# Kernel optimization log

Measured on AMD Instinct MI355X. Metric: run time of the kernel, lower is better.

Reference implementation:

```python
import jax, jax.numpy as jnp
import numpy as np

EPS = 1e-7  # K.epsilon()
ROUTINGS = 3
NUM_CAPSULE = 8
FILTERS = 16


def squash(v, axis=-1):
    s2 = jnp.sum(jnp.square(v), axis=axis, keepdims=True)
    scale = s2 / (1.0 + s2) / jnp.sqrt(s2 + EPS)
    return scale * v


def _conv_per_caps(x, w):
    # x: [B,H,W,Cin], w: [k,k,Cin,Cout]
    return jax.lax.conv_general_dilated(
        x, w, window_strides=(1, 1), padding='SAME',
        dimension_numbers=('NHWC', 'HWIO', 'NHWC'))


def setup_inputs() -> dict:
    key = jax.random.key(0)
    k1, k2 = jax.random.split(key, 2)
    B, H, Wd, IN_CAPS, IN_F = 32, 32, 32, 8, 16
    input_tensor = jax.random.normal(k1, (B, H, Wd, IN_CAPS, IN_F), dtype=jnp.float32)
    # he_normal fan_in = k*k*Cin = 3*3*16 = 144
    W = jax.random.normal(k2, (IN_CAPS, 3, 3, IN_F, NUM_CAPSULE * FILTERS), dtype=jnp.float32) * np.sqrt(2.0 / 144.0)
    b = jnp.full((1, 1, NUM_CAPSULE, FILTERS), 0.1, dtype=jnp.float32)
    return {"input_tensor": input_tensor, "W": W, "b": b}


def reference(input_tensor, W, b):
    B, H, Wd, in_caps, in_f = input_tensor.shape
    # per-input-capsule conv: vmap over capsule axis of input and weight
    votes = jax.vmap(_conv_per_caps, in_axes=(3, 0), out_axes=1)(input_tensor, W)
    # [B, in_caps, H, W, num_cap*F] -> [B, in_caps, H, W, num_cap, F]
    votes = votes.reshape(B, in_caps, H, Wd, NUM_CAPSULE, FILTERS)

    # dynamic routing
    logits = jnp.zeros((B, in_caps, H, Wd, NUM_CAPSULE), dtype=votes.dtype)
    activation = None
    for i in range(ROUTINGS):
        route = jax.nn.softmax(logits, axis=-1)  # over output capsules
        # sum over input capsules of route-weighted votes, plus bias
        preactivate = jnp.einsum('bihwc,bihwcf->bhwcf', route, votes) + b
        activation = squash(preactivate, axis=-1)
        if i < ROUTINGS - 1:
            # scalar-product agreement
            logits = logits + jnp.einsum('bihwcf,bhwcf->bihwc', votes, activation)
    return activation.astype(jnp.float32)
```

## Files before the change

### kernel.cpp

```cpp
#include <hip/hip_runtime.h>
#include <math.h>


typedef _Float16 fp16x8 __attribute__((ext_vector_type(8)));
typedef float f32x4 __attribute__((ext_vector_type(4)));

#define EPS 1e-7f
constexpr int PSTRIDE = 136;
constexpr int PCOLS   = 34;
constexpr int PROWS   = 4;
constexpr int LSTRIDE = 76;
constexpr int PXS     = 76;
constexpr int W_ELEMS = 40 * 8 * 64 * 8;

__device__ __forceinline__ float sumquad(float v) {
    v += __shfl_xor(v, 16);
    v += __shfl_xor(v, 32);
    return v;
}

__global__ __launch_bounds__(256)
void prep_weights(const float* __restrict__ wts,
                  _Float16* __restrict__ w16) {
    int n = blockIdx.x * 256 + threadIdx.x;
    if (n >= W_ELEMS) return;
    int j    = n & 7;
    int ln   = (n >> 3) & 63;
    int c0   = (n >> 9) & 7;
    int iq   = n >> 12;
    int i0   = iq / 5;
    int q0   = iq - i0 * 5;
    int k = q0 * 32 + (ln >> 4) * 8 + j;
    float w = 0.f;
    if (k < 144) w = wts[(i0 * 144 + k) * 128 + c0 * 16 + (ln & 15)];
    w16[n] = (_Float16)w;
}

__global__ __launch_bounds__(1024, 4)
void capsule_mfma_kernel(const float* __restrict__ x,
                         const _Float16* __restrict__ w16,
                         const float* __restrict__ bias,
                         float* __restrict__ out)
{
    __shared__ _Float16 patch[PROWS * PCOLS * PSTRIDE];
    __shared__ float lg_arr[64 * LSTRIDE];
    __shared__ float r_arr[64 * PXS];

    const int tid  = threadIdx.x;
    const int lane = tid & 63;
    const int w    = tid >> 6;
    const int c    = w & 7;
    const int g    = w >> 3;
    const int l15  = lane & 15;
    const int quad = lane >> 4;
    const int lane8 = lane * 8;

    const int bid = blockIdx.x;
    const int h2 = bid & 15, b = bid >> 4;
    const int h = h2 << 1;

    const float4* x4 = (const float4*)x;
    for (int idx = tid; idx < PROWS * PCOLS * 32; idx += 1024) {
        int ch4  = idx & 31;
        int slot = idx >> 5;
        int row  = slot / PCOLS;
        int colp = slot - row * PCOLS;
        int gh = h - 1 + row;
        int gw = colp - 1;
        float4 v = {0.f, 0.f, 0.f, 0.f};
        if ((unsigned)gh < 32u && (unsigned)gw < 32u)
            v = x4[(((b * 32 + gh) * 32 + gw) << 5) + ch4];
        _Float16 ph[4];
        ph[0] = (_Float16)v.x; ph[1] = (_Float16)v.y;
        ph[2] = (_Float16)v.z; ph[3] = (_Float16)v.w;
        *(ushort4*)&patch[slot * PSTRIDE + ch4 * 4] = *(const ushort4*)ph;
    }
    __syncthreads();

    int a_off[5];
    #pragma unroll
    for (int q = 0; q < 5; ++q) {
        int tap = 2 * q + (quad >> 1);
        if (tap > 8) tap = 8;
        int dy = tap / 3, dx = tap - dy * 3;
        a_off[q] = ((g + dy) * PCOLS + l15 + dx) * PSTRIDE + (quad & 1) * 8;
    }

    f32x4 acc[2][8];
    #pragma unroll
    for (int mt = 0; mt < 2; ++mt)
        #pragma unroll
        for (int i = 0; i < 8; ++i) acc[mt][i] = (f32x4){0.f, 0.f, 0.f, 0.f};

    #pragma unroll
    for (int q = 0; q < 5; ++q) {
        #pragma unroll
        for (int i = 0; i < 8; ++i) {
            int woff = ((i * 5 + q) * 8 + c) * 512 + lane8;
            fp16x8 aw = *(const fp16x8*)(w16 + woff);
            fp16x8 b0 = *(const fp16x8*)(patch + a_off[q] + i * 16);
            fp16x8 b1 = *(const fp16x8*)(patch + a_off[q] + 16 * PSTRIDE + i * 16);
            acc[0][i] = __builtin_amdgcn_mfma_f32_16x16x32_f16(aw, b0, acc[0][i], 0, 0, 0);
            acc[1][i] = __builtin_amdgcn_mfma_f32_16x16x32_f16(aw, b1, acc[1][i], 0, 0, 0);
        }
    }

    const float4 bb4 = *(const float4*)(bias + c * 16 + quad * 4);
    const float barr[4] = {bb4.x, bb4.y, bb4.z, bb4.w};

    float actv[2][4];

    #pragma unroll
    for (int mt = 0; mt < 2; ++mt) {
        float pre[4];
        #pragma unroll
        for (int r = 0; r < 4; ++r) {
            float s = acc[mt][0][r] + acc[mt][1][r] + acc[mt][2][r] + acc[mt][3][r]
                    + acc[mt][4][r] + acc[mt][5][r] + acc[mt][6][r] + acc[mt][7][r];
            pre[r] = s * 0.125f + barr[r];
        }
        float s2 = sumquad(pre[0]*pre[0] + pre[1]*pre[1] + pre[2]*pre[2] + pre[3]*pre[3]);
        float scale = s2 * __builtin_amdgcn_rsqf(s2 + EPS) * __builtin_amdgcn_rcpf(1.f + s2);
        #pragma unroll
        for (int r = 0; r < 4; ++r) actv[mt][r] = scale * pre[r];
    }
    #pragma unroll
    for (int mt = 0; mt < 2; ++mt) {
        int slot = g * 32 + mt * 16 + l15;
        #pragma unroll
        for (int i = 0; i < 8; ++i) {
            float t = acc[mt][i][0]*actv[mt][0] + acc[mt][i][1]*actv[mt][1]
                    + acc[mt][i][2]*actv[mt][2] + acc[mt][i][3]*actv[mt][3];
            t = sumquad(t);
            if (quad == 0) lg_arr[slot * LSTRIDE + i * 9 + c] = t;
        }
    }
    __syncthreads();
    if (tid < 512) {
        int p = tid >> 3, ii = tid & 7;
        const float* lrow = &lg_arr[p * LSTRIDE + ii * 9];
        float m = lrow[0];
        #pragma unroll
        for (int cc = 1; cc < 8; ++cc) m = fmaxf(m, lrow[cc]);
        float e[8]; float den = 0.f;
        #pragma unroll
        for (int cc = 0; cc < 8; ++cc) { e[cc] = __expf(lrow[cc] - m); den += e[cc]; }
        float rd = __builtin_amdgcn_rcpf(den);
        #pragma unroll
        for (int cc = 0; cc < 8; ++cc) r_arr[p * PXS + cc * 8 + ii] = e[cc] * rd;
    }
    __syncthreads();

    #pragma unroll
    for (int mt = 0; mt < 2; ++mt) {
        int slot = g * 32 + mt * 16 + l15;
        const float4* rp = (const float4*)&r_arr[slot * PXS + c * 8];
        float4 r0 = rp[0], r1 = rp[1];
        float pre[4];
        #pragma unroll
        for (int r = 0; r < 4; ++r) {
            float s;
            s  = r0.x * acc[mt][0][r]; s = fmaf(r0.y, acc[mt][1][r], s);
            s  = fmaf(r0.z, acc[mt][2][r], s); s = fmaf(r0.w, acc[mt][3][r], s);
            s  = fmaf(r1.x, acc[mt][4][r], s); s = fmaf(r1.y, acc[mt][5][r], s);
            s  = fmaf(r1.z, acc[mt][6][r], s); s = fmaf(r1.w, acc[mt][7][r], s);
            pre[r] = s + barr[r];
        }
        float s2 = sumquad(pre[0]*pre[0] + pre[1]*pre[1] + pre[2]*pre[2] + pre[3]*pre[3]);
        float scale = s2 * __builtin_amdgcn_rsqf(s2 + EPS) * __builtin_amdgcn_rcpf(1.f + s2);
        #pragma unroll
        for (int r = 0; r < 4; ++r) actv[mt][r] = scale * pre[r];
    }
    #pragma unroll
    for (int mt = 0; mt < 2; ++mt) {
        int slot = g * 32 + mt * 16 + l15;
        #pragma unroll
        for (int i = 0; i < 8; ++i) {
            float t = acc[mt][i][0]*actv[mt][0] + acc[mt][i][1]*actv[mt][1]
                    + acc[mt][i][2]*actv[mt][2] + acc[mt][i][3]*actv[mt][3];
            t = sumquad(t);
            if (quad == 0) lg_arr[slot * LSTRIDE + i * 9 + c] += t;
        }
    }
    __syncthreads();
    if (tid < 512) {
        int p = tid >> 3, ii = tid & 7;
        const float* lrow = &lg_arr[p * LSTRIDE + ii * 9];
        float m = lrow[0];
        #pragma unroll
        for (int cc = 1; cc < 8; ++cc) m = fmaxf(m, lrow[cc]);
        float e[8]; float den = 0.f;
        #pragma unroll
        for (int cc = 0; cc < 8; ++cc) { e[cc] = __expf(lrow[cc] - m); den += e[cc]; }
        float rd = __builtin_amdgcn_rcpf(den);
        #pragma unroll
        for (int cc = 0; cc < 8; ++cc) r_arr[p * PXS + cc * 8 + ii] = e[cc] * rd;
    }
    __syncthreads();

    #pragma unroll
    for (int mt = 0; mt < 2; ++mt) {
        int slot = g * 32 + mt * 16 + l15;
        const float4* rp = (const float4*)&r_arr[slot * PXS + c * 8];
        float4 r0 = rp[0], r1 = rp[1];
        float pre[4];
        #pragma unroll
        for (int r = 0; r < 4; ++r) {
            float s;
            s  = r0.x * acc[mt][0][r]; s = fmaf(r0.y, acc[mt][1][r], s);
            s  = fmaf(r0.z, acc[mt][2][r], s); s = fmaf(r0.w, acc[mt][3][r], s);
            s  = fmaf(r1.x, acc[mt][4][r], s); s = fmaf(r1.y, acc[mt][5][r], s);
            s  = fmaf(r1.z, acc[mt][6][r], s); s = fmaf(r1.w, acc[mt][7][r], s);
            pre[r] = s + barr[r];
        }
        float s2 = sumquad(pre[0]*pre[0] + pre[1]*pre[1] + pre[2]*pre[2] + pre[3]*pre[3]);
        float scale = s2 * __builtin_amdgcn_rsqf(s2 + EPS) * __builtin_amdgcn_rcpf(1.f + s2);
        float4 o4 = { scale*pre[0], scale*pre[1], scale*pre[2], scale*pre[3] };
        int gh = h + g;
        int px = mt * 16 + l15;
        *(float4*)(out + (((b * 32 + gh) * 32 + px) << 7) + c * 16 + quad * 4) = o4;
    }
}

extern "C" void kernel_launch(void* const* d_in, const int* in_sizes, int n_in,
                              void* d_out, int out_size, void* d_ws, size_t ws_size,
                              hipStream_t stream) {
    const float* x    = (const float*)d_in[0];
    const float* wts  = (const float*)d_in[1];
    const float* bias = (const float*)d_in[2];
    float* out        = (float*)d_out;
    _Float16* w16     = (_Float16*)d_ws;

    prep_weights<<<dim3(640), dim3(256), 0, stream>>>(wts, w16);
    capsule_mfma_kernel<<<dim3(512), dim3(1024), 0, stream>>>(x, w16, bias, out);
}
```

Before: 102.0 us.

## Process two row-pairs per block and prefetch the next input patch into LDS

Each block now handles two consecutive row-pairs, halving the grid. While the MFMA conv and routing for the first tile run, the input patch for the second tile is loaded from global memory straight into a new fp32 LDS staging buffer with global_load_lds. That staged data is then converted to fp16 for the second pass. The extra staging buffer greatly raises LDS use, which likely drops residency to one 1024-thread block per CU and so loses the overlap that came from running two blocks at once.

```diff
diff --git a/kernel.cpp b/kernel.cpp
--- a/kernel.cpp
+++ b/kernel.cpp
@@ -9,6 +9,7 @@
 constexpr int PSTRIDE = 136;
 constexpr int PCOLS   = 34;
 constexpr int PROWS   = 4;
+constexpr int NSTG    = PROWS * PCOLS * 32;
 constexpr int LSTRIDE = 76;
 constexpr int PXS     = 76;
 constexpr int W_ELEMS = 40 * 8 * 64 * 8;
@@ -17,6 +18,12 @@
     v += __shfl_xor(v, 16);
     v += __shfl_xor(v, 32);
     return v;
+}
+
+__device__ __forceinline__ void gll16(const float4* g, float4* l) {
+    __builtin_amdgcn_global_load_lds(
+        (const __attribute__((address_space(1))) unsigned int*)(const void*)g,
+        (__attribute__((address_space(3))) unsigned int*)(void*)l, 16, 0, 0);
 }
 
 __global__ __launch_bounds__(256)
@@ -43,6 +50,7 @@
                          float* __restrict__ out)
 {
     __shared__ _Float16 patch[PROWS * PCOLS * PSTRIDE];
+    __shared__ float4 stage32[NSTG];
     __shared__ float lg_arr[64 * LSTRIDE];
     __shared__ float r_arr[64 * PXS];
 
@@ -56,26 +64,12 @@
     const int lane8 = lane * 8;
 
     const int bid = blockIdx.x;
-    const int h2 = bid & 15, b = bid >> 4;
-    const int h = h2 << 1;
+    const int t0  = bid * 2;
+    const int h2  = t0 & 15;
+    const int b   = t0 >> 4;
+    const int h0  = h2 << 1;
 
     const float4* x4 = (const float4*)x;
-    for (int idx = tid; idx < PROWS * PCOLS * 32; idx += 1024) {
-        int ch4  = idx & 31;
-        int slot = idx >> 5;
-        int row  = slot / PCOLS;
-        int colp = slot - row * PCOLS;
-        int gh = h - 1 + row;
-        int gw = colp - 1;
-        float4 v = {0.f, 0.f, 0.f, 0.f};
-        if ((unsigned)gh < 32u && (unsigned)gw < 32u)
-            v = x4[(((b * 32 + gh) * 32 + gw) << 5) + ch4];
-        _Float16 ph[4];
-        ph[0] = (_Float16)v.x; ph[1] = (_Float16)v.y;
-        ph[2] = (_Float16)v.z; ph[3] = (_Float16)v.w;
-        *(ushort4*)&patch[slot * PSTRIDE + ch4 * 4] = *(const ushort4*)ph;
-    }
-    __syncthreads();
 
     int a_off[5];
     #pragma unroll
@@ -86,139 +80,194 @@
         a_off[q] = ((g + dy) * PCOLS + l15 + dx) * PSTRIDE + (quad & 1) * 8;
     }
 
-    f32x4 acc[2][8];
-    #pragma unroll
-    for (int mt = 0; mt < 2; ++mt)
-        #pragma unroll
-        for (int i = 0; i < 8; ++i) acc[mt][i] = (f32x4){0.f, 0.f, 0.f, 0.f};
-
-    #pragma unroll
-    for (int q = 0; q < 5; ++q) {
-        #pragma unroll
-        for (int i = 0; i < 8; ++i) {
-            int woff = ((i * 5 + q) * 8 + c) * 512 + lane8;
-            fp16x8 aw = *(const fp16x8*)(w16 + woff);
-            fp16x8 b0 = *(const fp16x8*)(patch + a_off[q] + i * 16);
-            fp16x8 b1 = *(const fp16x8*)(patch + a_off[q] + 16 * PSTRIDE + i * 16);
-            acc[0][i] = __builtin_amdgcn_mfma_f32_16x16x32_f16(aw, b0, acc[0][i], 0, 0, 0);
-            acc[1][i] = __builtin_amdgcn_mfma_f32_16x16x32_f16(aw, b1, acc[1][i], 0, 0, 0);
-        }
-    }
-
     const float4 bb4 = *(const float4*)(bias + c * 16 + quad * 4);
     const float barr[4] = {bb4.x, bb4.y, bb4.z, bb4.w};
 
-    float actv[2][4];
-
-    #pragma unroll
-    for (int mt = 0; mt < 2; ++mt) {
-        float pre[4];
-        #pragma unroll
-        for (int r = 0; r < 4; ++r) {
-            float s = acc[mt][0][r] + acc[mt][1][r] + acc[mt][2][r] + acc[mt][3][r]
-                    + acc[mt][4][r] + acc[mt][5][r] + acc[mt][6][r] + acc[mt][7][r];
-            pre[r] = s * 0.125f + barr[r];
-        }
-        float s2 = sumquad(pre[0]*pre[0] + pre[1]*pre[1] + pre[2]*pre[2] + pre[3]*pre[3]);
-        float scale = s2 * __builtin_amdgcn_rsqf(s2 + EPS) * __builtin_amdgcn_rcpf(1.f + s2);
-        #pragma unroll
-        for (int r = 0; r < 4; ++r) actv[mt][r] = scale * pre[r];
-    }
-    #pragma unroll
-    for (int mt = 0; mt < 2; ++mt) {
-        int slot = g * 32 + mt * 16 + l15;
-        #pragma unroll
-        for (int i = 0; i < 8; ++i) {
-            float t = acc[mt][i][0]*actv[mt][0] + acc[mt][i][1]*actv[mt][1]
-                    + acc[mt][i][2]*actv[mt][2] + acc[mt][i][3]*actv[mt][3];
-            t = sumquad(t);
-            if (quad == 0) lg_arr[slot * LSTRIDE + i * 9 + c] = t;
-        }
-    }
-    __syncthreads();
-    if (tid < 512) {
-        int p = tid >> 3, ii = tid & 7;
-        const float* lrow = &lg_arr[p * LSTRIDE + ii * 9];
-        float m = lrow[0];
-        #pragma unroll
-        for (int cc = 1; cc < 8; ++cc) m = fmaxf(m, lrow[cc]);
-        float e[8]; float den = 0.f;
-        #pragma unroll
-        for (int cc = 0; cc < 8; ++cc) { e[cc] = __expf(lrow[cc] - m); den += e[cc]; }
-        float rd = __builtin_amdgcn_rcpf(den);
-        #pragma unroll
-        for (int cc = 0; cc < 8; ++cc) r_arr[p * PXS + cc * 8 + ii] = e[cc] * rd;
-    }
-    __syncthreads();
-
-    #pragma unroll
-    for (int mt = 0; mt < 2; ++mt) {
-        int slot = g * 32 + mt * 16 + l15;
-        const float4* rp = (const float4*)&r_arr[slot * PXS + c * 8];
-        float4 r0 = rp[0], r1 = rp[1];
-        float pre[4];
-        #pragma unroll
-        for (int r = 0; r < 4; ++r) {
-            float s;
-            s  = r0.x * acc[mt][0][r]; s = fmaf(r0.y, acc[mt][1][r], s);
-            s  = fmaf(r0.z, acc[mt][2][r], s); s = fmaf(r0.w, acc[mt][3][r], s);
-            s  = fmaf(r1.x, acc[mt][4][r], s); s = fmaf(r1.y, acc[mt][5][r], s);
-            s  = fmaf(r1.z, acc[mt][6][r], s); s = fmaf(r1.w, acc[mt][7][r], s);
-            pre[r] = s + barr[r];
-        }
-        float s2 = sumquad(pre[0]*pre[0] + pre[1]*pre[1] + pre[2]*pre[2] + pre[3]*pre[3]);
-        float scale = s2 * __builtin_amdgcn_rsqf(s2 + EPS) * __builtin_amdgcn_rcpf(1.f + s2);
-        #pragma unroll
-        for (int r = 0; r < 4; ++r) actv[mt][r] = scale * pre[r];
-    }
-    #pragma unroll
-    for (int mt = 0; mt < 2; ++mt) {
-        int slot = g * 32 + mt * 16 + l15;
-        #pragma unroll
-        for (int i = 0; i < 8; ++i) {
-            float t = acc[mt][i][0]*actv[mt][0] + acc[mt][i][1]*actv[mt][1]
-                    + acc[mt][i][2]*actv[mt][2] + acc[mt][i][3]*actv[mt][3];
-            t = sumquad(t);
-            if (quad == 0) lg_arr[slot * LSTRIDE + i * 9 + c] += t;
-        }
-    }
-    __syncthreads();
-    if (tid < 512) {
-        int p = tid >> 3, ii = tid & 7;
-        const float* lrow = &lg_arr[p * LSTRIDE + ii * 9];
-        float m = lrow[0];
-        #pragma unroll
-        for (int cc = 1; cc < 8; ++cc) m = fmaxf(m, lrow[cc]);
-        float e[8]; float den = 0.f;
-        #pragma unroll
-        for (int cc = 0; cc < 8; ++cc) { e[cc] = __expf(lrow[cc] - m); den += e[cc]; }
-        float rd = __builtin_amdgcn_rcpf(den);
-        #pragma unroll
-        for (int cc = 0; cc < 8; ++cc) r_arr[p * PXS + cc * 8 + ii] = e[cc] * rd;
-    }
-    __syncthreads();
-
-    #pragma unroll
-    for (int mt = 0; mt < 2; ++mt) {
-        int slot = g * 32 + mt * 16 + l15;
-        const float4* rp = (const float4*)&r_arr[slot * PXS + c * 8];
-        float4 r0 = rp[0], r1 = rp[1];
-        float pre[4];
-        #pragma unroll
-        for (int r = 0; r < 4; ++r) {
-            float s;
-            s  = r0.x * acc[mt][0][r]; s = fmaf(r0.y, acc[mt][1][r], s);
-            s  = fmaf(r0.z, acc[mt][2][r], s); s = fmaf(r0.w, acc[mt][3][r], s);
-            s  = fmaf(r1.x, acc[mt][4][r], s); s = fmaf(r1.y, acc[mt][5][r], s);
-            s  = fmaf(r1.z, acc[mt][6][r], s); s = fmaf(r1.w, acc[mt][7][r], s);
-            pre[r] = s + barr[r];
-        }
-        float s2 = sumquad(pre[0]*pre[0] + pre[1]*pre[1] + pre[2]*pre[2] + pre[3]*pre[3]);
-        float scale = s2 * __builtin_amdgcn_rsqf(s2 + EPS) * __builtin_amdgcn_rcpf(1.f + s2);
-        float4 o4 = { scale*pre[0], scale*pre[1], scale*pre[2], scale*pre[3] };
-        int gh = h + g;
-        int px = mt * 16 + l15;
-        *(float4*)(out + (((b * 32 + gh) * 32 + px) << 7) + c * 16 + quad * 4) = o4;
+    for (int s = 0; s < 2; ++s) {
+        const int h = h0 + 2 * s;
+
+        if (s == 0) {
+            for (int idx = tid; idx < NSTG; idx += 1024) {
+                int ch4  = idx & 31;
+                int slot = idx >> 5;
+                int row  = slot / PCOLS;
+                int colp = slot - row * PCOLS;
+                int gh = h - 1 + row;
+                int gw = colp - 1;
+                float4 v = {0.f, 0.f, 0.f, 0.f};
+                if ((unsigned)gh < 32u && (unsigned)gw < 32u)
+                    v = x4[(((b * 32 + gh) * 32 + gw) << 5) + ch4];
+                _Float16 ph[4];
+                ph[0] = (_Float16)v.x; ph[1] = (_Float16)v.y;
+                ph[2] = (_Float16)v.z; ph[3] = (_Float16)v.w;
+                *(ushort4*)&patch[slot * PSTRIDE + ch4 * 4] = *(const ushort4*)ph;
+            }
+        } else {
+            for (int idx = tid; idx < NSTG; idx += 1024) {
+                int ch4  = idx & 31;
+                int slot = idx >> 5;
+                int row  = slot / PCOLS;
+                int colp = slot - row * PCOLS;
+                int gh = h - 1 + row;
+                int gw = colp - 1;
+                float4 v = {0.f, 0.f, 0.f, 0.f};
+                if ((unsigned)gh < 32u && (unsigned)gw < 32u)
+                    v = stage32[idx];
+                _Float16 ph[4];
+                ph[0] = (_Float16)v.x; ph[1] = (_Float16)v.y;
+                ph[2] = (_Float16)v.z; ph[3] = (_Float16)v.w;
+                *(ushort4*)&patch[slot * PSTRIDE + ch4 * 4] = *(const ushort4*)ph;
+            }
+        }
+        __syncthreads();
+
+        f32x4 acc[2][8];
+        #pragma unroll
+        for (int mt = 0; mt < 2; ++mt)
+            #pragma unroll
+            for (int i = 0; i < 8; ++i) acc[mt][i] = (f32x4){0.f, 0.f, 0.f, 0.f};
+
+        #pragma unroll
+        for (int q = 0; q < 5; ++q) {
+            #pragma unroll
+            for (int i = 0; i < 8; ++i) {
+                int woff = ((i * 5 + q) * 8 + c) * 512 + lane8;
+                fp16x8 aw = *(const fp16x8*)(w16 + woff);
+                fp16x8 b0 = *(const fp16x8*)(patch + a_off[q] + i * 16);
+                fp16x8 b1 = *(const fp16x8*)(patch + a_off[q] + 16 * PSTRIDE + i * 16);
+                acc[0][i] = __builtin_amdgcn_mfma_f32_16x16x32_f16(aw, b0, acc[0][i], 0, 0, 0);
+                acc[1][i] = __builtin_amdgcn_mfma_f32_16x16x32_f16(aw, b1, acc[1][i], 0, 0, 0);
+            }
+        }
+
+        if (s == 0) {
+            const int h1 = h0 + 2;
+            for (int idx = tid; idx < NSTG; idx += 1024) {
+                int ch4  = idx & 31;
+                int slot = idx >> 5;
+                int row  = slot / PCOLS;
+                int colp = slot - row * PCOLS;
+                int gh = h1 - 1 + row;
+                int gw = colp - 1;
+                int sgh = ((unsigned)gh < 32u) ? gh : 0;
+                int sgw = ((unsigned)gw < 32u) ? gw : 0;
+                const float4* src = x4 + ((((b * 32 + sgh) * 32 + sgw) << 5) + ch4);
+                gll16(src, stage32 + (idx - lane));
+            }
+        }
+
+        float actv[2][4];
+
+        #pragma unroll
+        for (int mt = 0; mt < 2; ++mt) {
+            float pre[4];
+            #pragma unroll
+            for (int r = 0; r < 4; ++r) {
+                float ss = acc[mt][0][r] + acc[mt][1][r] + acc[mt][2][r] + acc[mt][3][r]
+                         + acc[mt][4][r] + acc[mt][5][r] + acc[mt][6][r] + acc[mt][7][r];
+                pre[r] = ss * 0.125f + barr[r];
+            }
+            float s2 = sumquad(pre[0]*pre[0] + pre[1]*pre[1] + pre[2]*pre[2] + pre[3]*pre[3]);
+            float scale = s2 * __builtin_amdgcn_rsqf(s2 + EPS) * __builtin_amdgcn_rcpf(1.f + s2);
+            #pragma unroll
+            for (int r = 0; r < 4; ++r) actv[mt][r] = scale * pre[r];
+        }
+        #pragma unroll
+        for (int mt = 0; mt < 2; ++mt) {
+            int slot = g * 32 + mt * 16 + l15;
+            #pragma unroll
+            for (int i = 0; i < 8; ++i) {
+                float t = acc[mt][i][0]*actv[mt][0] + acc[mt][i][1]*actv[mt][1]
+                        + acc[mt][i][2]*actv[mt][2] + acc[mt][i][3]*actv[mt][3];
+                t = sumquad(t);
+                if (quad == 0) lg_arr[slot * LSTRIDE + i * 9 + c] = t;
+            }
+        }
+        __syncthreads();
+        if (tid < 512) {
+            int p = tid >> 3, ii = tid & 7;
+            const float* lrow = &lg_arr[p * LSTRIDE + ii * 9];
+            float m = lrow[0];
+            #pragma unroll
+            for (int cc = 1; cc < 8; ++cc) m = fmaxf(m, lrow[cc]);
+            float e[8]; float den = 0.f;
+            #pragma unroll
+            for (int cc = 0; cc < 8; ++cc) { e[cc] = __expf(lrow[cc] - m); den += e[cc]; }
+            float rd = __builtin_amdgcn_rcpf(den);
+            #pragma unroll
+            for (int cc = 0; cc < 8; ++cc) r_arr[p * PXS + cc * 8 + ii] = e[cc] * rd;
+        }
+        __syncthreads();
+
+        #pragma unroll
+        for (int mt = 0; mt < 2; ++mt) {
+            int slot = g * 32 + mt * 16 + l15;
+            const float4* rp = (const float4*)&r_arr[slot * PXS + c * 8];
+            float4 r0 = rp[0], r1 = rp[1];
+            float pre[4];
+            #pragma unroll
+            for (int r = 0; r < 4; ++r) {
+                float ss;
+                ss = r0.x * acc[mt][0][r]; ss = fmaf(r0.y, acc[mt][1][r], ss);
+                ss = fmaf(r0.z, acc[mt][2][r], ss); ss = fmaf(r0.w, acc[mt][3][r], ss);
+                ss = fmaf(r1.x, acc[mt][4][r], ss); ss = fmaf(r1.y, acc[mt][5][r], ss);
+                ss = fmaf(r1.z, acc[mt][6][r], ss); ss = fmaf(r1.w, acc[mt][7][r], ss);
+                pre[r] = ss + barr[r];
+            }
+            float s2 = sumquad(pre[0]*pre[0] + pre[1]*pre[1] + pre[2]*pre[2] + pre[3]*pre[3]);
+            float scale = s2 * __builtin_amdgcn_rsqf(s2 + EPS) * __builtin_amdgcn_rcpf(1.f + s2);
+            #pragma unroll
+            for (int r = 0; r < 4; ++r) actv[mt][r] = scale * pre[r];
+        }
+        #pragma unroll
+        for (int mt = 0; mt < 2; ++mt) {
+            int slot = g * 32 + mt * 16 + l15;
+            #pragma unroll
+            for (int i = 0; i < 8; ++i) {
+                float t = acc[mt][i][0]*actv[mt][0] + acc[mt][i][1]*actv[mt][1]
+                        + acc[mt][i][2]*actv[mt][2] + acc[mt][i][3]*actv[mt][3];
+                t = sumquad(t);
+                if (quad == 0) lg_arr[slot * LSTRIDE + i * 9 + c] += t;
+            }
+        }
+        __syncthreads();
+        if (tid < 512) {
+            int p = tid >> 3, ii = tid & 7;
+            const float* lrow = &lg_arr[p * LSTRIDE + ii * 9];
+            float m = lrow[0];
+            #pragma unroll
+            for (int cc = 1; cc < 8; ++cc) m = fmaxf(m, lrow[cc]);
+            float e[8]; float den = 0.f;
+            #pragma unroll
+            for (int cc = 0; cc < 8; ++cc) { e[cc] = __expf(lrow[cc] - m); den += e[cc]; }
+            float rd = __builtin_amdgcn_rcpf(den);
+            #pragma unroll
+            for (int cc = 0; cc < 8; ++cc) r_arr[p * PXS + cc * 8 + ii] = e[cc] * rd;
+        }
+        __syncthreads();
+
+        #pragma unroll
+        for (int mt = 0; mt < 2; ++mt) {
+            int slot = g * 32 + mt * 16 + l15;
+            const float4* rp = (const float4*)&r_arr[slot * PXS + c * 8];
+            float4 r0 = rp[0], r1 = rp[1];
+            float pre[4];
+            #pragma unroll
+            for (int r = 0; r < 4; ++r) {
+                float ss;
+                ss = r0.x * acc[mt][0][r]; ss = fmaf(r0.y, acc[mt][1][r], ss);
+                ss = fmaf(r0.z, acc[mt][2][r], ss); ss = fmaf(r0.w, acc[mt][3][r], ss);
+                ss = fmaf(r1.x, acc[mt][4][r], ss); ss = fmaf(r1.y, acc[mt][5][r], ss);
+                ss = fmaf(r1.z, acc[mt][6][r], ss); ss = fmaf(r1.w, acc[mt][7][r], ss);
+                pre[r] = ss + barr[r];
+            }
+            float s2 = sumquad(pre[0]*pre[0] + pre[1]*pre[1] + pre[2]*pre[2] + pre[3]*pre[3]);
+            float scale = s2 * __builtin_amdgcn_rsqf(s2 + EPS) * __builtin_amdgcn_rcpf(1.f + s2);
+            float4 o4 = { scale*pre[0], scale*pre[1], scale*pre[2], scale*pre[3] };
+            int gh = h + g;
+            int px = mt * 16 + l15;
+            *(float4*)(out + (((b * 32 + gh) * 32 + px) << 7) + c * 16 + quad * 4) = o4;
+        }
     }
 }
 
@@ -232,5 +281,5 @@
     _Float16* w16     = (_Float16*)d_ws;
 
     prep_weights<<<dim3(640), dim3(256), 0, stream>>>(wts, w16);
-    capsule_mfma_kernel<<<dim3(512), dim3(1024), 0, stream>>>(x, w16, bias, out);
-}
+    capsule_mfma_kernel<<<dim3(256), dim3(1024), 0, stream>>>(x, w16, bias, out);
+}
```

Result: slower. 158.9 us (+55.8%).
